# Kernel tuning notes

Hardware: AMD Instinct MI355X
Metric: run time of the kernel (lower is better)

## Reference

```python
import jax, jax.numpy as jnp
import numpy as np

NEG = -1000000.0  # mask fill value used by the torch module


def setup_inputs() -> dict:
    key = jax.random.key(0)
    kq, kk, kv, km = jax.random.split(key, 4)
    B, Q, K, D = 8, 2048, 2048, 128
    queries = jax.random.normal(kq, (B, Q, D), dtype=jnp.float32)
    keys = jax.random.normal(kk, (B, K, D), dtype=jnp.float32)
    values = jax.random.normal(kv, (B, K, D), dtype=jnp.float32)
    attntion_mask = jax.random.randint(km, (B, K), 0, 2, dtype=jnp.int32)
    return {"queries": queries, "keys": keys, "values": values,
            "attntion_mask": attntion_mask}


def reference(queries, keys, values, attntion_mask):
    d = queries.shape[-1]
    # scores: [B, Q, K]
    scores = jnp.einsum('bqd,bkd->bqk', queries, keys) / jnp.sqrt(
        jnp.asarray(d, dtype=queries.dtype))
    # 2D mask [B, K] broadcasts over the query axis (torch repeat_interleave)
    mask = attntion_mask.astype(bool)[:, None, :]  # [B, 1, K]
    scores = jnp.where(mask, scores, NEG)
    weights = jax.nn.softmax(scores, axis=-1)
    # dropout rate is 0.0 (eval mode) -> identity
    return jnp.einsum('bqk,bkv->bqv', weights, values)
```

## Files before the change

kernel.cpp:

```cpp
#include <hip/hip_runtime.h>
#include <stdint.h>

typedef __attribute__((ext_vector_type(8))) short short8;
typedef __attribute__((ext_vector_type(4))) float f32x4;

#define NB 8
#define NQ 2048
#define NK 2048
#define ND 128
#define SCALE 0.08838834764831845f
#define L2E   1.4426950408889634f
#define FMAXC 10.0f

__device__ __forceinline__ uint32_t pk_bf16(float a, float b) {
  uint32_t ua = __builtin_bit_cast(uint32_t, a);
  uint32_t ub = __builtin_bit_cast(uint32_t, b);
  ua += 0x7FFFu + ((ua >> 16) & 1u);
  ub += 0x7FFFu + ((ub >> 16) & 1u);
  return (ua >> 16) | (ub & 0xFFFF0000u);
}

__device__ __forceinline__ void dma16(const void* g, void* l) {
  __builtin_amdgcn_global_load_lds((const __attribute__((address_space(1))) void*)g,
                                   (__attribute__((address_space(3))) void*)l, 16, 0, 0);
}

__global__ __launch_bounds__(256) void compact_kernel(const int* __restrict__ maskm,
                                                      int* __restrict__ idxArr,
                                                      int* __restrict__ KcArr) {
  __shared__ int cnt;
  const int b = blockIdx.x;
  const int t = threadIdx.x;
  const int lane = t & 63;
  if (t == 0) cnt = 0;
  __syncthreads();
#pragma unroll
  for (int j = 0; j < 8; ++j) {
    int k = t * 8 + j;
    bool bit = maskm[b * NK + k] != 0;
    unsigned long long m = __ballot(bit);
    int pre = __popcll(m & ((1ull << lane) - 1ull));
    int tot = __popcll(m);
    int base = 0;
    if (lane == 0 && tot) base = atomicAdd(&cnt, tot);
    base = __shfl(base, 0);
    if (bit) idxArr[b * NK + base + pre] = k;
  }
  __syncthreads();
  int kc = cnt;
  for (int s = kc + t; s < NK; s += 256) idxArr[b * NK + s] = -1;
  if (t == 0) KcArr[b] = kc;
}

__global__ __launch_bounds__(256) void prep_kernel(const float* __restrict__ v,
                                                   const float* __restrict__ kin,
                                                   ushort* __restrict__ vt,
                                                   ushort* __restrict__ kb,
                                                   const int* __restrict__ idxArr) {
  const int t = threadIdx.x;
  const int bid = blockIdx.x;
  if (bid < 512) {
    __shared__ __align__(16) float tile[4096];
    char* sm = (char*)tile;
    const int b = bid >> 6;
    const int k0 = ((bid >> 1) & 31) << 6;
    const int d0 = (bid & 1) << 6;
#pragma unroll
    for (int i = 0; i < 4; ++i) {
      int id = i * 256 + t;
      int k = id >> 4, c = id & 15;
      int src = idxArr[b * NK + k0 + k];
      uint4 val; val.x = 0u; val.y = 0u; val.z = 0u; val.w = 0u;
      if (src >= 0) val = *(const uint4*)(v + (size_t)(b * NK + src) * ND + d0 + c * 4);
      *(uint4*)(sm + k * 256 + ((c ^ (k & 15)) * 16)) = val;
    }
    __syncthreads();
#pragma unroll
    for (int i = 0; i < 2; ++i) {
      int id = i * 256 + t;
      int d = id >> 3, kc = id & 7;
      uint32_t w[4];
#pragma unroll
      for (int jj = 0; jj < 4; ++jj) {
        int kA = kc * 8 + jj * 2, kB = kA + 1;
        float fa = *(const float*)(sm + kA * 256 + (((d >> 2) ^ (kA & 15)) * 16) + (d & 3) * 4);
        float fb = *(const float*)(sm + kB * 256 + (((d >> 2) ^ (kB & 15)) * 16) + (d & 3) * 4);
        w[jj] = pk_bf16(fa, fb);
      }
      uint4 o; o.x = w[0]; o.y = w[1]; o.z = w[2]; o.w = w[3];
      *(uint4*)(vt + (size_t)(b * ND + d0 + d) * NK + k0 + kc * 8) = o;
    }
  } else {
    int gs = (bid - 512) * 16 + (t >> 4);
    int src = idxArr[gs];
    int col = (t & 15) * 8;
    uint4 u; u.x = 0u; u.y = 0u; u.z = 0u; u.w = 0u;
    if (src >= 0) {
      int b2 = gs >> 11;
      const float* p = kin + (size_t)(b2 * NK + src) * ND + col;
      f32x4 a = *(const f32x4*)p;
      f32x4 c = *(const f32x4*)(p + 4);
      u.x = pk_bf16(a[0], a[1]); u.y = pk_bf16(a[2], a[3]);
      u.z = pk_bf16(c[0], c[1]); u.w = pk_bf16(c[2], c[3]);
    }
    *(uint4*)(kb + (size_t)gs * ND + col) = u;
  }
}

template <bool MASKED>
__device__ __forceinline__ void do_softmax(const f32x4 st[2], float& l_,
                                           char* pbase, int r, int quad, int rem) {
  const float C1 = SCALE * L2E;
  const float C2 = -FMAXC * L2E;
  float p[2][4]; float ps = 0.f;
#pragma unroll
  for (int mt = 0; mt < 2; ++mt) {
    float t0 = fmaf(st[mt][0], C1, C2);
    float t1 = fmaf(st[mt][1], C1, C2);
    float t2 = fmaf(st[mt][2], C1, C2);
    float t3 = fmaf(st[mt][3], C1, C2);
    if (MASKED) {
      const int rm = rem - mt * 16;
      t0 = (rm > 0) ? t0 : -2.0e6f;
      t1 = (rm > 1) ? t1 : -2.0e6f;
      t2 = (rm > 2) ? t2 : -2.0e6f;
      t3 = (rm > 3) ? t3 : -2.0e6f;
    }
    p[mt][0] = exp2f(t0); p[mt][1] = exp2f(t1);
    p[mt][2] = exp2f(t2); p[mt][3] = exp2f(t3);
    ps += p[mt][0] + p[mt][1] + p[mt][2] + p[mt][3];
  }
  l_ += ps;
#pragma unroll
  for (int mt = 0; mt < 2; ++mt) {
    uint2 w; w.x = pk_bf16(p[mt][0], p[mt][1]); w.y = pk_bf16(p[mt][2], p[mt][3]);
    *(uint2*)(pbase + r * 64 + (((mt * 4 + quad) ^ (r & 6)) * 8)) = w;
  }
}

#define LDS_BYTES 106496
__global__ __launch_bounds__(512) void attn_kernel(const float* __restrict__ qm,
                                                   const ushort* __restrict__ kbm,
                                                   const ushort* __restrict__ vtm,
                                                   const int* __restrict__ KcArr,
                                                   ushort* __restrict__ opart,
                                                   float* __restrict__ lpart) {
  __shared__ __align__(16) char sm[LDS_BYTES];
  const int o   = blockIdx.x;
  const int bid = (o & 7) * 32 + (o >> 3);
  const int b   = bid >> 5;
  const int q0  = ((bid >> 1) & 15) << 7;
  const int spl = bid & 1;
  const int t = threadIdx.x;
  const int lane = t & 63;
  const int wave = t >> 6;
  const int r = lane & 15;
  const int quad = lane >> 4;
  const int half = wave >> 2;
  const int qg = wave & 3;

  const int Kc   = KcArr[b];
  const int n_it = (Kc + 127) >> 7;
  const int CH   = n_it << 5;

  uint32_t koff[2], voff[2];
#pragma unroll
  for (int j = 0; j < 2; ++j) {
    int i = wave * 2 + j;
    int rho = i * 4 + (lane >> 4);
    int ck = (lane & 15) ^ (rho & 15);
    int krow = (spl * 2 + (rho >> 5)) * CH + (rho & 31);
    koff[j] = (uint32_t)(b * NK + krow) * ND + ck * 8;
    int rv = i * 16 + (lane >> 2);
    int cv = (lane & 3) ^ (rv & 3);
    voff[j] = (uint32_t)(b * ND + (rv & 127)) * NK + (spl * 2 + (rv >> 7)) * CH + cv * 8;
  }

#define ISSUE_TILE(tt, bufi)                                                    \
  {                                                                             \
    const uint32_t kadd_ = (uint32_t)(tt) * 32 * ND;                            \
    const uint32_t vadd_ = (uint32_t)(tt) * 32;                                 \
    char* kb_ = sm + (bufi) * 16384;                                            \
    char* vb_ = sm + 49152 + (bufi) * 16384;                                    \
    _Pragma("unroll")                                                           \
    for (int j = 0; j < 2; ++j) {                                               \
      dma16(kbm + koff[j] + kadd_, kb_ + (wave * 2 + j) * 1024);                \
      dma16(vtm + voff[j] + vadd_, vb_ + (wave * 2 + j) * 1024);                \
    }                                                                           \
  }

  f32x4 qraw[2][4][2];
#pragma unroll
  for (int qt = 0; qt < 2; ++qt)
#pragma unroll
    for (int ks = 0; ks < 4; ++ks) {
      const float* p = qm + (size_t)(b * NQ + q0 + qg * 32 + qt * 16 + r) * ND + ks * 32 + quad * 8;
      qraw[qt][ks][0] = *(const f32x4*)p;
      qraw[qt][ks][1] = *(const f32x4*)(p + 4);
    }
  ISSUE_TILE(0, 0);
  if (n_it > 1) ISSUE_TILE(1, 1);
  short8 qf[2][4];
#pragma unroll
  for (int qt = 0; qt < 2; ++qt)
#pragma unroll
    for (int ks = 0; ks < 4; ++ks) {
      uint4 u;
      u.x = pk_bf16(qraw[qt][ks][0][0], qraw[qt][ks][0][1]);
      u.y = pk_bf16(qraw[qt][ks][0][2], qraw[qt][ks][0][3]);
      u.z = pk_bf16(qraw[qt][ks][1][0], qraw[qt][ks][1][1]);
      u.w = pk_bf16(qraw[qt][ks][1][2], qraw[qt][ks][1][3]);
      qf[qt][ks] = __builtin_bit_cast(short8, u);
    }

  f32x4 oacc[2][8];
#pragma unroll
  for (int qt = 0; qt < 2; ++qt)
#pragma unroll
    for (int dt = 0; dt < 8; ++dt) oacc[qt][dt] = (f32x4){0.f, 0.f, 0.f, 0.f};
  float l_[2] = {0.f, 0.f};

  char* const pbase = sm + 98304 + wave * 1024;

  const int vlim0 = Kc - (spl * 2 + half) * CH;

  int cur = 0;
  for (int it = 0; it < n_it; ++it) {
    if (it < n_it - 1) asm volatile("s_waitcnt vmcnt(4)" ::: "memory");
    else               asm volatile("s_waitcnt vmcnt(0)" ::: "memory");
    __builtin_amdgcn_sched_barrier(0);
    __builtin_amdgcn_s_barrier();
    __builtin_amdgcn_sched_barrier(0);

    if (it + 2 < n_it) {
      int b2 = cur + 2; if (b2 >= 3) b2 -= 3;
      ISSUE_TILE(it + 2, b2);
    }

    char* const kcur = sm + cur * 16384;
    char* const vcur = sm + 49152 + cur * 16384;

    f32x4 st[2][2];
#pragma unroll
    for (int mt = 0; mt < 2; ++mt) {
      short8 kf[4];
#pragma unroll
      for (int ks = 0; ks < 4; ++ks)
        kf[ks] = *(const short8*)(kcur + half * 8192 + (mt * 16 + r) * 256 + (((ks * 4 + quad) ^ r) * 16));
#pragma unroll
      for (int qt = 0; qt < 2; ++qt) {
        f32x4 acc = (f32x4){0.f, 0.f, 0.f, 0.f};
#pragma unroll
        for (int ks = 0; ks < 4; ++ks)
          acc = __builtin_amdgcn_mfma_f32_16x16x32_bf16(kf[ks], qf[qt][ks], acc, 0, 0, 0);
        st[mt][qt] = acc;
      }
    }

    const int vlim = vlim0 - it * 32;
    short8 pf[2];
#pragma unroll
    for (int qt = 0; qt < 2; ++qt) {
      f32x4 s2[2] = { st[0][qt], st[1][qt] };
      if (vlim >= 32) do_softmax<false>(s2, l_[qt], pbase, r, quad, 0);
      else            do_softmax<true >(s2, l_[qt], pbase, r, quad, vlim - quad * 4);
      pf[qt] = *(const short8*)(pbase + r * 64 + (((quad * 2) ^ (r & 6)) * 8));
    }

#pragma unroll
    for (int dt = 0; dt < 8; ++dt) {
      short8 vf = *(const short8*)(vcur + half * 8192 + (dt * 16 + r) * 64 + ((quad ^ (r & 3)) * 16));
#pragma unroll
      for (int qt = 0; qt < 2; ++qt)
        oacc[qt][dt] = __builtin_amdgcn_mfma_f32_16x16x32_bf16(vf, pf[qt], oacc[qt][dt], 0, 0, 0);
    }

    cur = (cur == 2) ? 0 : cur + 1;
  }

  __syncthreads();
  float* xch = (float*)(sm + qg * 17408) + lane * 68;
  if (half == 1) {
    xch[0] = l_[0]; xch[1] = l_[1];
#pragma unroll
    for (int qt = 0; qt < 2; ++qt)
#pragma unroll
      for (int dt = 0; dt < 8; ++dt)
        *(f32x4*)(xch + 4 + (qt * 8 + dt) * 4) = oacc[qt][dt];
  }
  __syncthreads();
  if (half == 0) {
#pragma unroll
    for (int qt = 0; qt < 2; ++qt) {
      const int qrow = b * NQ + q0 + qg * 32 + qt * 16 + r;
      float ls = l_[qt] + xch[qt];
      ls += __shfl_xor(ls, 16);
      ls += __shfl_xor(ls, 32);
      if (quad == 0) lpart[spl * NB * NQ + qrow] = ls;
#pragma unroll
      for (int dt = 0; dt < 8; ++dt) {
        f32x4 o1 = *(const f32x4*)(xch + 4 + (qt * 8 + dt) * 4);
        f32x4 ov = oacc[qt][dt] + o1;
        uint2 w; w.x = pk_bf16(ov[0], ov[1]); w.y = pk_bf16(ov[2], ov[3]);
        *(uint2*)(opart + (size_t)spl * NB * NQ * ND + (size_t)qrow * ND + dt * 16 + quad * 4) = w;
      }
    }
  }
#undef ISSUE_TILE
}

__global__ __launch_bounds__(256) void merge_kernel(const ushort* __restrict__ opart,
                                                    const float* __restrict__ lpart,
                                                    float* __restrict__ outm) {
  const int gid = blockIdx.x * 256 + threadIdx.x;
  const int row = gid >> 4;
  const int d0 = (gid & 15) << 3;
  const size_t off = (size_t)row * ND + d0;
  uint4 u0 = *(const uint4*)(opart + off);
  uint4 u1 = *(const uint4*)(opart + (size_t)NB * NQ * ND + off);
  float inv = 1.0f / (lpart[row] + lpart[NB * NQ + row]);
  f32x4 lo, hi;
  uint32_t w;
#define UP(u, dst0, dst1) w = (u); dst0 = __builtin_bit_cast(float, w << 16); \
                          dst1 = __builtin_bit_cast(float, w & 0xFFFF0000u);
  float a0,a1,b0,b1;
  UP(u0.x, a0, a1) UP(u1.x, b0, b1) lo[0] = (a0 + b0) * inv; lo[1] = (a1 + b1) * inv;
  UP(u0.y, a0, a1) UP(u1.y, b0, b1) lo[2] = (a0 + b0) * inv; lo[3] = (a1 + b1) * inv;
  UP(u0.z, a0, a1) UP(u1.z, b0, b1) hi[0] = (a0 + b0) * inv; hi[1] = (a1 + b1) * inv;
  UP(u0.w, a0, a1) UP(u1.w, b0, b1) hi[2] = (a0 + b0) * inv; hi[3] = (a1 + b1) * inv;
#undef UP
  *(f32x4*)(outm + off) = lo;
  *(f32x4*)(outm + off + 4) = hi;
}

extern "C" void kernel_launch(void* const* d_in, const int* in_sizes, int n_in,
                              void* d_out, int out_size, void* d_ws, size_t ws_size,
                              hipStream_t stream) {
  const float* q   = (const float*)d_in[0];
  const float* k   = (const float*)d_in[1];
  const float* v   = (const float*)d_in[2];
  const int*   msk = (const int*)d_in[3];
  float* out = (float*)d_out;
  ushort* kb = (ushort*)d_ws;
  ushort* vt = kb + (size_t)NB * NK * ND;
  ushort* op = vt + (size_t)NB * NK * ND;
  float*  lp = (float*)(op + 2 * (size_t)NB * NQ * ND);
  int* idxA  = (int*)(lp + 2 * (size_t)NB * NQ);
  int* kcA   = idxA + (size_t)NB * NK;

  compact_kernel<<<NB, 256, 0, stream>>>(msk, idxA, kcA);
  prep_kernel<<<1536, 256, 0, stream>>>(v, k, vt, kb, idxA);
  attn_kernel<<<256, 512, 0, stream>>>(q, kb, vt, kcA, op, lp);
  merge_kernel<<<1024, 256, 0, stream>>>(op, lp, out);
}
```

Baseline: 107.0 us.

## Split keys within block across four waves, drop split-K merge kernel

Each block now handles 64 query rows over the full compacted key range, with the four waves of each query group taking interleaved 32-key slices of a 128-key tile. Partial sums are reduced in LDS and the output is normalized and written directly in fp32, which removes the cross-block split, the bf16 partial buffers and the separate merge kernel launch. V is single-buffered and loaded each iteration behind an extra barrier, while K stays triple-buffered at double the size. LDS use rises to about 136 KB per block, and the added mid-iteration barrier may expose V load latency.

```diff
diff --git a/kernel.cpp b/kernel.cpp
--- a/kernel.cpp
+++ b/kernel.cpp
@@ -138,55 +138,54 @@
   }
 }
 
-#define LDS_BYTES 106496
+#define LDS_BYTES 139264
 __global__ __launch_bounds__(512) void attn_kernel(const float* __restrict__ qm,
                                                    const ushort* __restrict__ kbm,
                                                    const ushort* __restrict__ vtm,
                                                    const int* __restrict__ KcArr,
-                                                   ushort* __restrict__ opart,
-                                                   float* __restrict__ lpart) {
+                                                   float* __restrict__ outm) {
   __shared__ __align__(16) char sm[LDS_BYTES];
   const int o   = blockIdx.x;
   const int bid = (o & 7) * 32 + (o >> 3);
   const int b   = bid >> 5;
-  const int q0  = ((bid >> 1) & 15) << 7;
-  const int spl = bid & 1;
+  const int q0  = (bid & 31) << 6;
   const int t = threadIdx.x;
   const int lane = t & 63;
   const int wave = t >> 6;
   const int r = lane & 15;
   const int quad = lane >> 4;
-  const int half = wave >> 2;
-  const int qg = wave & 3;
+  const int qg = wave >> 2;
+  const int kq = wave & 3;
 
   const int Kc   = KcArr[b];
   const int n_it = (Kc + 127) >> 7;
-  const int CH   = n_it << 5;
-
-  uint32_t koff[2], voff[2];
-#pragma unroll
-  for (int j = 0; j < 2; ++j) {
-    int i = wave * 2 + j;
+
+  uint32_t koff[4], voff[4];
+#pragma unroll
+  for (int j = 0; j < 4; ++j) {
+    int i = wave * 4 + j;
     int rho = i * 4 + (lane >> 4);
     int ck = (lane & 15) ^ (rho & 15);
-    int krow = (spl * 2 + (rho >> 5)) * CH + (rho & 31);
-    koff[j] = (uint32_t)(b * NK + krow) * ND + ck * 8;
-    int rv = i * 16 + (lane >> 2);
-    int cv = (lane & 3) ^ (rv & 3);
-    voff[j] = (uint32_t)(b * ND + (rv & 127)) * NK + (spl * 2 + (rv >> 7)) * CH + cv * 8;
-  }
-
-#define ISSUE_TILE(tt, bufi)                                                    \
+    koff[j] = (uint32_t)(b * NK + rho) * ND + ck * 8;
+    int u = i * 16 + (lane >> 2);
+    int cv = (lane & 3) ^ (u & 3);
+    voff[j] = (uint32_t)(b * ND + (u & 127)) * NK + (u >> 7) * 32 + cv * 8;
+  }
+
+#define ISSUE_K(tt, bufi)                                                       \
   {                                                                             \
-    const uint32_t kadd_ = (uint32_t)(tt) * 32 * ND;                            \
-    const uint32_t vadd_ = (uint32_t)(tt) * 32;                                 \
-    char* kb_ = sm + (bufi) * 16384;                                            \
-    char* vb_ = sm + 49152 + (bufi) * 16384;                                    \
+    const uint32_t kadd_ = (uint32_t)(tt) * 128 * ND;                           \
+    char* kb_ = sm + (bufi) * 32768;                                            \
     _Pragma("unroll")                                                           \
-    for (int j = 0; j < 2; ++j) {                                               \
-      dma16(kbm + koff[j] + kadd_, kb_ + (wave * 2 + j) * 1024);                \
-      dma16(vtm + voff[j] + vadd_, vb_ + (wave * 2 + j) * 1024);                \
-    }                                                                           \
+    for (int j = 0; j < 4; ++j)                                                 \
+      dma16(kbm + koff[j] + kadd_, kb_ + (wave * 4 + j) * 1024);                \
+  }
+#define ISSUE_V(tt)                                                             \
+  {                                                                             \
+    const uint32_t vadd_ = (uint32_t)(tt) * 128;                                \
+    _Pragma("unroll")                                                           \
+    for (int j = 0; j < 4; ++j)                                                 \
+      dma16(vtm + voff[j] + vadd_, sm + 98304 + (wave * 4 + j) * 1024);         \
   }
 
   f32x4 qraw[2][4][2];
@@ -198,8 +197,8 @@
       qraw[qt][ks][0] = *(const f32x4*)p;
       qraw[qt][ks][1] = *(const f32x4*)(p + 4);
     }
-  ISSUE_TILE(0, 0);
-  if (n_it > 1) ISSUE_TILE(1, 1);
+  ISSUE_K(0, 0);
+  if (n_it > 1) ISSUE_K(1, 1);
   short8 qf[2][4];
 #pragma unroll
   for (int qt = 0; qt < 2; ++qt)
@@ -220,25 +219,24 @@
     for (int dt = 0; dt < 8; ++dt) oacc[qt][dt] = (f32x4){0.f, 0.f, 0.f, 0.f};
   float l_[2] = {0.f, 0.f};
 
-  char* const pbase = sm + 98304 + wave * 1024;
-
-  const int vlim0 = Kc - (spl * 2 + half) * CH;
+  char* const pbase = sm + 131072 + wave * 1024;
+  char* const vbuf  = sm + 98304 + kq * 8192;
 
   int cur = 0;
   for (int it = 0; it < n_it; ++it) {
-    if (it < n_it - 1) asm volatile("s_waitcnt vmcnt(4)" ::: "memory");
+    if (it + 1 < n_it) asm volatile("s_waitcnt vmcnt(4)" ::: "memory");
     else               asm volatile("s_waitcnt vmcnt(0)" ::: "memory");
     __builtin_amdgcn_sched_barrier(0);
     __builtin_amdgcn_s_barrier();
     __builtin_amdgcn_sched_barrier(0);
 
+    ISSUE_V(it);
     if (it + 2 < n_it) {
       int b2 = cur + 2; if (b2 >= 3) b2 -= 3;
-      ISSUE_TILE(it + 2, b2);
-    }
-
-    char* const kcur = sm + cur * 16384;
-    char* const vcur = sm + 49152 + cur * 16384;
+      ISSUE_K(it + 2, b2);
+    }
+
+    char* const kcur = sm + cur * 32768 + kq * 8192;
 
     f32x4 st[2][2];
 #pragma unroll
@@ -246,7 +244,7 @@
       short8 kf[4];
 #pragma unroll
       for (int ks = 0; ks < 4; ++ks)
-        kf[ks] = *(const short8*)(kcur + half * 8192 + (mt * 16 + r) * 256 + (((ks * 4 + quad) ^ r) * 16));
+        kf[ks] = *(const short8*)(kcur + (mt * 16 + r) * 256 + (((ks * 4 + quad) ^ r) * 16));
 #pragma unroll
       for (int qt = 0; qt < 2; ++qt) {
         f32x4 acc = (f32x4){0.f, 0.f, 0.f, 0.f};
@@ -257,7 +255,7 @@
       }
     }
 
-    const int vlim = vlim0 - it * 32;
+    const int vlim = Kc - it * 128 - kq * 32;
     short8 pf[2];
 #pragma unroll
     for (int qt = 0; qt < 2; ++qt) {
@@ -267,9 +265,15 @@
       pf[qt] = *(const short8*)(pbase + r * 64 + (((quad * 2) ^ (r & 6)) * 8));
     }
 
+    if (it + 2 < n_it) asm volatile("s_waitcnt vmcnt(4)" ::: "memory");
+    else               asm volatile("s_waitcnt vmcnt(0)" ::: "memory");
+    __builtin_amdgcn_sched_barrier(0);
+    __builtin_amdgcn_s_barrier();
+    __builtin_amdgcn_sched_barrier(0);
+
 #pragma unroll
     for (int dt = 0; dt < 8; ++dt) {
-      short8 vf = *(const short8*)(vcur + half * 8192 + (dt * 16 + r) * 64 + ((quad ^ (r & 3)) * 16));
+      short8 vf = *(const short8*)(vbuf + (dt * 16 + r) * 64 + ((quad ^ (r & 3)) * 16));
 #pragma unroll
       for (int qt = 0; qt < 2; ++qt)
         oacc[qt][dt] = __builtin_amdgcn_mfma_f32_16x16x32_bf16(vf, pf[qt], oacc[qt][dt], 0, 0, 0);
@@ -279,8 +283,8 @@
   }
 
   __syncthreads();
-  float* xch = (float*)(sm + qg * 17408) + lane * 68;
-  if (half == 1) {
+  if (kq != 0) {
+    float* xch = (float*)(sm + (qg * 3 + (kq - 1)) * 17408) + lane * 68;
     xch[0] = l_[0]; xch[1] = l_[1];
 #pragma unroll
     for (int qt = 0; qt < 2; ++qt)
@@ -289,48 +293,33 @@
         *(f32x4*)(xch + 4 + (qt * 8 + dt) * 4) = oacc[qt][dt];
   }
   __syncthreads();
-  if (half == 0) {
+  if (kq == 0) {
+    float* x0 = (float*)(sm + (qg * 3 + 0) * 17408) + lane * 68;
+    float* x1 = (float*)(sm + (qg * 3 + 1) * 17408) + lane * 68;
+    float* x2 = (float*)(sm + (qg * 3 + 2) * 17408) + lane * 68;
 #pragma unroll
     for (int qt = 0; qt < 2; ++qt) {
       const int qrow = b * NQ + q0 + qg * 32 + qt * 16 + r;
-      float ls = l_[qt] + xch[qt];
+      float ls = l_[qt] + x0[qt] + x1[qt] + x2[qt];
       ls += __shfl_xor(ls, 16);
       ls += __shfl_xor(ls, 32);
-      if (quad == 0) lpart[spl * NB * NQ + qrow] = ls;
+      float inv = 1.0f / ls;
 #pragma unroll
       for (int dt = 0; dt < 8; ++dt) {
-        f32x4 o1 = *(const f32x4*)(xch + 4 + (qt * 8 + dt) * 4);
-        f32x4 ov = oacc[qt][dt] + o1;
-        uint2 w; w.x = pk_bf16(ov[0], ov[1]); w.y = pk_bf16(ov[2], ov[3]);
-        *(uint2*)(opart + (size_t)spl * NB * NQ * ND + (size_t)qrow * ND + dt * 16 + quad * 4) = w;
+        f32x4 o1 = *(const f32x4*)(x0 + 4 + (qt * 8 + dt) * 4);
+        f32x4 o2 = *(const f32x4*)(x1 + 4 + (qt * 8 + dt) * 4);
+        f32x4 o3 = *(const f32x4*)(x2 + 4 + (qt * 8 + dt) * 4);
+        f32x4 ov = oacc[qt][dt];
+        ov[0] = (ov[0] + o1[0] + o2[0] + o3[0]) * inv;
+        ov[1] = (ov[1] + o1[1] + o2[1] + o3[1]) * inv;
+        ov[2] = (ov[2] + o1[2] + o2[2] + o3[2]) * inv;
+        ov[3] = (ov[3] + o1[3] + o2[3] + o3[3]) * inv;
+        *(f32x4*)(outm + (size_t)qrow * ND + dt * 16 + quad * 4) = ov;
       }
     }
   }
-#undef ISSUE_TILE
-}
-
-__global__ __launch_bounds__(256) void merge_kernel(const ushort* __restrict__ opart,
-                                                    const float* __restrict__ lpart,
-                                                    float* __restrict__ outm) {
-  const int gid = blockIdx.x * 256 + threadIdx.x;
-  const int row = gid >> 4;
-  const int d0 = (gid & 15) << 3;
-  const size_t off = (size_t)row * ND + d0;
-  uint4 u0 = *(const uint4*)(opart + off);
-  uint4 u1 = *(const uint4*)(opart + (size_t)NB * NQ * ND + off);
-  float inv = 1.0f / (lpart[row] + lpart[NB * NQ + row]);
-  f32x4 lo, hi;
-  uint32_t w;
-#define UP(u, dst0, dst1) w = (u); dst0 = __builtin_bit_cast(float, w << 16); \
-                          dst1 = __builtin_bit_cast(float, w & 0xFFFF0000u);
-  float a0,a1,b0,b1;
-  UP(u0.x, a0, a1) UP(u1.x, b0, b1) lo[0] = (a0 + b0) * inv; lo[1] = (a1 + b1) * inv;
-  UP(u0.y, a0, a1) UP(u1.y, b0, b1) lo[2] = (a0 + b0) * inv; lo[3] = (a1 + b1) * inv;
-  UP(u0.z, a0, a1) UP(u1.z, b0, b1) hi[0] = (a0 + b0) * inv; hi[1] = (a1 + b1) * inv;
-  UP(u0.w, a0, a1) UP(u1.w, b0, b1) hi[2] = (a0 + b0) * inv; hi[3] = (a1 + b1) * inv;
-#undef UP
-  *(f32x4*)(outm + off) = lo;
-  *(f32x4*)(outm + off + 4) = hi;
+#undef ISSUE_K
+#undef ISSUE_V
 }
 
 extern "C" void kernel_launch(void* const* d_in, const int* in_sizes, int n_in,
@@ -343,13 +332,10 @@
   float* out = (float*)d_out;
   ushort* kb = (ushort*)d_ws;
   ushort* vt = kb + (size_t)NB * NK * ND;
-  ushort* op = vt + (size_t)NB * NK * ND;
-  float*  lp = (float*)(op + 2 * (size_t)NB * NQ * ND);
-  int* idxA  = (int*)(lp + 2 * (size_t)NB * NQ);
+  int* idxA  = (int*)(vt + (size_t)NB * NK * ND);
   int* kcA   = idxA + (size_t)NB * NK;
 
   compact_kernel<<<NB, 256, 0, stream>>>(msk, idxA, kcA);
   prep_kernel<<<1536, 256, 0, stream>>>(v, k, vt, kb, idxA);
-  attn_kernel<<<256, 512, 0, stream>>>(q, kb, vt, kcA, op, lp);
-  merge_kernel<<<1024, 256, 0, stream>>>(op, lp, out);
-}
+  attn_kernel<<<256, 512, 0, stream>>>(q, kb, vt, kcA, out);
+}
```

Measured after the change: 105.0 us. About the same (-1.9%).
